# Performance work log

Hardware: AMD Instinct MI355X
Metric: run time of the kernel (lower is better)

Reference implementation:

```python
import jax, jax.numpy as jnp
import numpy as np

EEG_CH = 64      # eeg_channel_new
WIN = 128        # window_length
KEN = 10         # cnn_ken_num
CONV_H = 64      # cnn_conv_hight (stride/kernel height)


def setup_inputs() -> dict:
    key = jax.random.key(0)
    ks = jax.random.split(key, 11)
    n = jax.random.normal
    return {
        "x": n(ks[0], (1, 1, 66, 128), dtype=jnp.float32),
        # SE fcn: Linear(64,64) -> Tanh -> Linear(64,64) -> Sigmoid -> Softmax
        "se_w1": n(ks[1], (64, 64), dtype=jnp.float32) * 0.1,
        "se_b1": n(ks[2], (64,), dtype=jnp.float32) * 0.1,
        "se_w2": n(ks[3], (64, 64), dtype=jnp.float32) * 0.1,
        "se_b2": n(ks[4], (64,), dtype=jnp.float32) * 0.1,
        # Conv2d(1, 10, (64, 9), stride=(64, 1))
        "conv_w": n(ks[5], (10, 1, 64, 9), dtype=jnp.float32) * 0.05,
        "conv_b": n(ks[6], (10,), dtype=jnp.float32) * 0.05,
        # fcn: Linear(20,10) -> Sigmoid -> Linear(10,2) -> Softmax
        "fcn_w1": n(ks[7], (10, 20), dtype=jnp.float32) * 0.1,
        "fcn_b1": n(ks[8], (10,), dtype=jnp.float32) * 0.1,
        "fcn_w2": n(ks[9], (2, 10), dtype=jnp.float32) * 0.1,
        "fcn_b2": n(ks[10], (2,), dtype=jnp.float32) * 0.1,
    }


def _dot(a, b):
    # Faithful to torch: tensordot over dim 0 -> [64,1]; diag of non-square -> [1];
    # then broadcast-divide by per-column norms -> [64].
    temp = jnp.diagonal(jnp.tensordot(a, b, axes=[[0], [0]]))  # [1]
    norm_a = jnp.linalg.norm(a, axis=0)                        # [64]
    norm_b = jnp.linalg.norm(b, axis=0)                        # [1]
    return temp / (norm_a * norm_b)                            # [64]


def reference(x, se_w1, se_b1, se_w2, se_b2, conv_w, conv_b,
              fcn_w1, fcn_b1, fcn_w2, fcn_b2):
    eeg = x[:, :, 1:1 + EEG_CH, :]      # [1,1,64,128]
    wav_a = x[:, :, 0:1, :]             # [1,1,1,128]
    wav_b = x[:, :, -1:, :]             # [1,1,1,128]

    e2 = eeg.reshape(EEG_CH, WIN)       # [64,128]
    r_a = _dot(e2.T, wav_a.reshape(1, WIN).T)   # [64]
    r_b = _dot(e2.T, wav_b.reshape(1, WIN).T)   # [64]
    eeg_r = jnp.concatenate([r_a, r_b]).reshape(2, -1)  # [2,64]

    # SE channel attention
    h = jnp.tanh(eeg_r @ se_w1.T + se_b1)
    se_w = jax.nn.softmax(jax.nn.sigmoid(h @ se_w2.T + se_b2), axis=1)  # [2,64]
    sd = eeg.reshape(1, EEG_CH, WIN).transpose(1, 0, 2)  # [64,1,128]
    sd = jnp.concatenate([sd, sd], axis=0)               # [128,1,128]
    # (transpose(0,2) * w.view(1,-1)).transpose(0,2) == scale along doubled-channel dim
    eeg_se = (sd * se_w.reshape(-1)[:, None, None]).transpose(1, 0, 2)  # [1,128,128]

    y = eeg_se.reshape(1, 1, 2 * EEG_CH, WIN)            # [1,1,128,128]
    y = jax.lax.conv_general_dilated(
        y, conv_w, window_strides=(CONV_H, 1), padding='VALID',
        dimension_numbers=('NCHW', 'OIHW', 'NCHW'))       # [1,10,2,120]
    y = jax.nn.relu(y + conv_b[None, :, None, None])
    # AdaptiveAvgPool2d((2,1)): H already 2, mean over W
    y = jnp.mean(y, axis=3, keepdims=True)                # [1,10,2,1]
    y = y.reshape(1, -1)                                  # [1,20]

    h2 = jax.nn.sigmoid(y @ fcn_w1.T + fcn_b1)
    return jax.nn.softmax(h2 @ fcn_w2.T + fcn_b2, axis=1)  # [1,2]
```

## Files before the change

kernel.cpp:

```cpp
#include <hip/hip_runtime.h>
#include <math.h>

#define EEG_CH 64
#define WIN    128
#define KW     9
#define OUTW   120
#define NOUT   10
#define ROWP   132
#define CWP    12

__device__ float        g_msum[2 * NOUT];
__device__ unsigned int g_ctr = 0;

__device__ __forceinline__ float readlane_f(float v, int l) {
    return __int_as_float(__builtin_amdgcn_readlane(__float_as_int(v), l));
}

__launch_bounds__(1024)
__global__ void cnn_fused(const float* __restrict__ xg,
                          const float* __restrict__ w1g, const float* __restrict__ b1g,
                          const float* __restrict__ w2g, const float* __restrict__ b2g,
                          const float* __restrict__ cwg, const float* __restrict__ cbg,
                          const float* __restrict__ f1w, const float* __restrict__ f1b,
                          const float* __restrict__ f2w, const float* __restrict__ f2b,
                          float* __restrict__ out)
{
    __shared__ float w1l[64 * 64];
    __shared__ float w2l[64 * 64];
    __shared__ float xl[64 * ROWP];
    __shared__ float cwl[64 * CWP];
    __shared__ float rnorm[66];
    __shared__ float nums[2];
    __shared__ float sef[128];
    __shared__ float part[8][2][OUTW];
    __shared__ float msh[2];
    __shared__ int   sflag;
    __shared__ float msums[2 * NOUT];
    __shared__ float fcnl[232];

    const int tid  = threadIdx.x;
    const int wv   = tid >> 6;
    const int lane = tid & 63;
    const int o    = blockIdx.x;

    const int chbase = (wv & 7) * 8;

    if (tid < 576) {
        const float v = cwg[o * (EEG_CH * KW) + tid];
        cwl[(tid / KW) * CWP + (tid % KW)] = v;
    } else if (tid < 808) {
        const int t = tid - 576;
        float v;
        if      (t < 200) v = f1w[t];
        else if (t < 210) v = f1b[t - 200];
        else if (t < 230) v = f2w[t - 210];
        else              v = f2b[t - 230];
        fcnl[t] = v;
    }
    for (int t = tid; t < 2048; t += 1024) {
        const int row = t >> 5, c4 = t & 31;
        const float4 v = *(const float4*)(xg + (row + 1) * WIN + c4 * 4);
        *(float4*)(xl + row * ROWP + c4 * 4) = v;
    }
    for (int t = tid; t < 2048; t += 1024) {
        const int j  = t & 63;
        const int i4 = (t >> 6) & 15;
        const float* __restrict__ src = (t < 1024) ? w1g : w2g;
        float* __restrict__ dst = (t < 1024) ? w1l : w2l;
        const float4 v = *(const float4*)(src + j * 64 + i4 * 4);
        dst[(i4 * 4 + 0) * 64 + j] = v.x;
        dst[(i4 * 4 + 1) * 64 + j] = v.y;
        dst[(i4 * 4 + 2) * 64 + j] = v.z;
        dst[(i4 * 4 + 3) * 64 + j] = v.w;
    }
    for (int row = wv; row < 66; row += 16) {
        const float v0 = xg[row * WIN + lane];
        const float v1 = xg[row * WIN + 64 + lane];
        float s = v0 * v0 + v1 * v1;
        for (int off = 32; off > 0; off >>= 1) s += __shfl_xor(s, off, 64);
        if (lane == 0) rnorm[row] = sqrtf(s);
    }
    if (wv < 2) {
        const int wrow = (wv == 0) ? 0 : 65;
        float p = xg[WIN + lane]      * xg[wrow * WIN + lane]
                + xg[WIN + 64 + lane] * xg[wrow * WIN + 64 + lane];
        for (int off = 32; off > 0; off >>= 1) p += __shfl_xor(p, off, 64);
        if (lane == 0) nums[wv] = p;
    }
    __syncthreads();

    const int wbase = (lane < 60) ? 2 * lane : 116;
    float p0a[8], p1a[8];
    if (wv < 8) {
        #pragma unroll
        for (int ii = 0; ii < 8; ++ii) {
            const int i = chbase + ii;
            const float2* xp = (const float2*)(xl + i * ROWP + wbase);
            const float2 x0 = xp[0], x1 = xp[1], x2 = xp[2], x3 = xp[3], x4 = xp[4];
            const float xw[10] = { x0.x, x0.y, x1.x, x1.y, x2.x, x2.y,
                                   x3.x, x3.y, x4.x, x4.y };
            const float4 wa = *(const float4*)(cwl + i * CWP);
            const float4 wb = *(const float4*)(cwl + i * CWP + 4);
            const float  w8 = cwl[i * CWP + 8];
            const float wk[KW] = { wa.x, wa.y, wa.z, wa.w,
                                   wb.x, wb.y, wb.z, wb.w, w8 };
            float p0 = 0.f, p1 = 0.f;
            #pragma unroll
            for (int k = 0; k < KW; ++k) {
                p0 += xw[k]     * wk[k];
                p1 += xw[k + 1] * wk[k];
            }
            p0a[ii] = p0;
            p1a[ii] = p1;
        }
    } else if (wv < 10) {
        const int r = wv - 8, j = lane;
        const float er = nums[r] / (rnorm[j + 1] * (r == 0 ? rnorm[0] : rnorm[65]));
        float acc = b1g[j];
        #pragma unroll
        for (int i = 0; i < 64; ++i)
            acc += readlane_f(er, i) * w1l[i * 64 + j];
        const float hv = tanhf(acc);
        float acc2 = b2g[j];
        #pragma unroll
        for (int i = 0; i < 64; ++i)
            acc2 += readlane_f(hv, i) * w2l[i * 64 + j];
        const float sg = 1.f / (1.f + expf(-acc2));
        float mx = sg;
        for (int off = 32; off > 0; off >>= 1) mx = fmaxf(mx, __shfl_xor(mx, off, 64));
        const float e = expf(sg - mx);
        float ss = e;
        for (int off = 32; off > 0; off >>= 1) ss += __shfl_xor(ss, off, 64);
        sef[r * 64 + j] = e / ss;
    }
    __syncthreads();

    if (wv < 8) {
        float q00 = 0.f, q01 = 0.f;
        float q10 = 0.f, q11 = 0.f;
        #pragma unroll
        for (int ii = 0; ii < 8; ++ii) {
            const float s0 = sef[chbase + ii];
            const float s1 = sef[64 + chbase + ii];
            q00 += s0 * p0a[ii];  q01 += s0 * p1a[ii];
            q10 += s1 * p0a[ii];  q11 += s1 * p1a[ii];
        }
        if (lane < 60) {
            *(float2*)(&part[wv][0][wbase]) = make_float2(q00, q01);
            *(float2*)(&part[wv][1][wbase]) = make_float2(q10, q11);
        }
    }
    __syncthreads();

    if (wv < 2) {
        const float bo = cbg[o];
        float r = 0.f;
        if (lane < 60) {
            float v0 = part[0][wv][wbase], v1 = part[0][wv][wbase + 1];
            #pragma unroll
            for (int q = 1; q < 8; ++q) {
                v0 += part[q][wv][wbase];
                v1 += part[q][wv][wbase + 1];
            }
            v0 += bo; v1 += bo;
            r = fmaxf(v0, 0.f) + fmaxf(v1, 0.f);
        }
        for (int off = 32; off > 0; off >>= 1) r += __shfl_xor(r, off, 64);
        if (lane == 0) msh[wv] = r * (1.0f / OUTW);
    }
    __syncthreads();

    if (tid == 0) {
        __hip_atomic_store(&g_msum[o * 2 + 0], msh[0], __ATOMIC_RELAXED, __HIP_MEMORY_SCOPE_AGENT);
        __hip_atomic_store(&g_msum[o * 2 + 1], msh[1], __ATOMIC_RELAXED, __HIP_MEMORY_SCOPE_AGENT);
        const unsigned old = __hip_atomic_fetch_add(&g_ctr, 1u, __ATOMIC_ACQ_REL, __HIP_MEMORY_SCOPE_AGENT);
        sflag = (old % 10u == 9u) ? 1 : 0;
    }
    __syncthreads();

    if (sflag) {
        if (tid < 2 * NOUT)
            msums[tid] = __hip_atomic_load(&g_msum[tid], __ATOMIC_ACQUIRE, __HIP_MEMORY_SCOPE_AGENT);
        __syncthreads();
        if (tid < 64) {
            float h2v = 0.f;
            if (lane < 10) {
                float a = fcnl[200 + lane];
                #pragma unroll
                for (int p = 0; p < 20; ++p) a += msums[p] * fcnl[lane * 20 + p];
                h2v = 1.f / (1.f + expf(-a));
            }
            float t0 = (lane < 10) ? h2v * fcnl[210 + lane] : 0.f;
            float t1 = (lane < 10) ? h2v * fcnl[220 + lane] : 0.f;
            for (int off = 32; off > 0; off >>= 1) {
                t0 += __shfl_xor(t0, off, 64);
                t1 += __shfl_xor(t1, off, 64);
            }
            if (lane == 0) {
                const float l0 = fcnl[230] + t0, l1 = fcnl[231] + t1;
                const float m  = fmaxf(l0, l1);
                const float e0 = expf(l0 - m), e1 = expf(l1 - m);
                out[0] = e0 / (e0 + e1);
                out[1] = e1 / (e0 + e1);
            }
        }
    }
}

extern "C" void kernel_launch(void* const* d_in, const int* in_sizes, int n_in,
                              void* d_out, int out_size, void* d_ws, size_t ws_size,
                              hipStream_t stream) {
    (void)in_sizes; (void)n_in; (void)ws_size; (void)out_size; (void)d_ws;
    const float* xg  = (const float*)d_in[0];
    const float* w1  = (const float*)d_in[1];
    const float* b1  = (const float*)d_in[2];
    const float* w2  = (const float*)d_in[3];
    const float* b2  = (const float*)d_in[4];
    const float* cw  = (const float*)d_in[5];
    const float* cb  = (const float*)d_in[6];
    const float* f1w = (const float*)d_in[7];
    const float* f1b = (const float*)d_in[8];
    const float* f2w = (const float*)d_in[9];
    const float* f2b = (const float*)d_in[10];
    float* out = (float*)d_out;

    cnn_fused<<<dim3(NOUT), dim3(1024), 0, stream>>>(xg, w1, b1, w2, b2,
                                                     cw, cb, f1w, f1b, f2w, f2b, out);
}
```

Before: 82.90 us.

## Hold SE weights in registers and read conv input directly from global

The SE-branch waves now load their rows of the two 64x64 weight matrices straight into registers as float4s, so the transposed LDS staging of those matrices goes away. The conv waves read x windows directly from global or L1 instead of going through an LDS copy. Row-norm work is moved off the SE waves so their register loads can overlap it. Together these remove roughly 50KB of LDS traffic and staging stores, at the cost of 128 extra VGPRs per SE lane (possible spilling under the 1024-thread launch bound) and uncached-LDS global reads in the conv loop.

```diff
diff --git a/kernel.cpp b/kernel.cpp
--- a/kernel.cpp
+++ b/kernel.cpp
@@ -6,7 +6,6 @@
 #define KW     9
 #define OUTW   120
 #define NOUT   10
-#define ROWP   132
 #define CWP    12
 
 __device__ float        g_msum[2 * NOUT];
@@ -25,9 +24,6 @@
                           const float* __restrict__ f2w, const float* __restrict__ f2b,
                           float* __restrict__ out)
 {
-    __shared__ float w1l[64 * 64];
-    __shared__ float w2l[64 * 64];
-    __shared__ float xl[64 * ROWP];
     __shared__ float cwl[64 * CWP];
     __shared__ float rnorm[66];
     __shared__ float nums[2];
@@ -45,11 +41,24 @@
 
     const int chbase = (wv & 7) * 8;
 
-    if (tid < 576) {
-        const float v = cwg[o * (EEG_CH * KW) + tid];
-        cwl[(tid / KW) * CWP + (tid % KW)] = v;
-    } else if (tid < 808) {
-        const int t = tid - 576;
+    float4 w1r[16], w2r[16];
+    float  b1v = 0.f, b2v = 0.f;
+    if (wv == 8 || wv == 9) {
+        const float* __restrict__ r1 = w1g + lane * 64;
+        const float* __restrict__ r2 = w2g + lane * 64;
+        #pragma unroll
+        for (int q = 0; q < 16; ++q) w1r[q] = *(const float4*)(r1 + 4 * q);
+        #pragma unroll
+        for (int q = 0; q < 16; ++q) w2r[q] = *(const float4*)(r2 + 4 * q);
+        b1v = b1g[lane];
+        b2v = b2g[lane];
+    }
+    if (wv < 8) {
+        for (int t = tid; t < 576; t += 512)
+            cwl[(t / KW) * CWP + (t % KW)] = cwg[o * (EEG_CH * KW) + t];
+    }
+    if (tid >= 640 && tid < 872) {
+        const int t = tid - 640;
         float v;
         if      (t < 200) v = f1w[t];
         else if (t < 210) v = f1b[t - 200];
@@ -57,28 +66,15 @@
         else              v = f2b[t - 230];
         fcnl[t] = v;
     }
-    for (int t = tid; t < 2048; t += 1024) {
-        const int row = t >> 5, c4 = t & 31;
-        const float4 v = *(const float4*)(xg + (row + 1) * WIN + c4 * 4);
-        *(float4*)(xl + row * ROWP + c4 * 4) = v;
-    }
-    for (int t = tid; t < 2048; t += 1024) {
-        const int j  = t & 63;
-        const int i4 = (t >> 6) & 15;
-        const float* __restrict__ src = (t < 1024) ? w1g : w2g;
-        float* __restrict__ dst = (t < 1024) ? w1l : w2l;
-        const float4 v = *(const float4*)(src + j * 64 + i4 * 4);
-        dst[(i4 * 4 + 0) * 64 + j] = v.x;
-        dst[(i4 * 4 + 1) * 64 + j] = v.y;
-        dst[(i4 * 4 + 2) * 64 + j] = v.z;
-        dst[(i4 * 4 + 3) * 64 + j] = v.w;
-    }
-    for (int row = wv; row < 66; row += 16) {
-        const float v0 = xg[row * WIN + lane];
-        const float v1 = xg[row * WIN + 64 + lane];
-        float s = v0 * v0 + v1 * v1;
-        for (int off = 32; off > 0; off >>= 1) s += __shfl_xor(s, off, 64);
-        if (lane == 0) rnorm[row] = sqrtf(s);
+    if (wv < 8 || wv >= 10) {
+        const int wvn = (wv < 8) ? wv : wv - 2;
+        for (int row = wvn; row < 66; row += 14) {
+            const float v0 = xg[row * WIN + lane];
+            const float v1 = xg[row * WIN + 64 + lane];
+            float s = v0 * v0 + v1 * v1;
+            for (int off = 32; off > 0; off >>= 1) s += __shfl_xor(s, off, 64);
+            if (lane == 0) rnorm[row] = sqrtf(s);
+        }
     }
     if (wv < 2) {
         const int wrow = (wv == 0) ? 0 : 65;
@@ -95,7 +91,7 @@
         #pragma unroll
         for (int ii = 0; ii < 8; ++ii) {
             const int i = chbase + ii;
-            const float2* xp = (const float2*)(xl + i * ROWP + wbase);
+            const float2* xp = (const float2*)(xg + (i + 1) * WIN + wbase);
             const float2 x0 = xp[0], x1 = xp[1], x2 = xp[2], x3 = xp[3], x4 = xp[4];
             const float xw[10] = { x0.x, x0.y, x1.x, x1.y, x2.x, x2.y,
                                    x3.x, x3.y, x4.x, x4.y };
@@ -116,15 +112,25 @@
     } else if (wv < 10) {
         const int r = wv - 8, j = lane;
         const float er = nums[r] / (rnorm[j + 1] * (r == 0 ? rnorm[0] : rnorm[65]));
-        float acc = b1g[j];
-        #pragma unroll
-        for (int i = 0; i < 64; ++i)
-            acc += readlane_f(er, i) * w1l[i * 64 + j];
+        float acc = b1v;
+        #pragma unroll
+        for (int q = 0; q < 16; ++q) {
+            const float4 w = w1r[q];
+            acc += readlane_f(er, 4 * q + 0) * w.x;
+            acc += readlane_f(er, 4 * q + 1) * w.y;
+            acc += readlane_f(er, 4 * q + 2) * w.z;
+            acc += readlane_f(er, 4 * q + 3) * w.w;
+        }
         const float hv = tanhf(acc);
-        float acc2 = b2g[j];
-        #pragma unroll
-        for (int i = 0; i < 64; ++i)
-            acc2 += readlane_f(hv, i) * w2l[i * 64 + j];
+        float acc2 = b2v;
+        #pragma unroll
+        for (int q = 0; q < 16; ++q) {
+            const float4 w = w2r[q];
+            acc2 += readlane_f(hv, 4 * q + 0) * w.x;
+            acc2 += readlane_f(hv, 4 * q + 1) * w.y;
+            acc2 += readlane_f(hv, 4 * q + 2) * w.z;
+            acc2 += readlane_f(hv, 4 * q + 3) * w.w;
+        }
         const float sg = 1.f / (1.f + expf(-acc2));
         float mx = sg;
         for (int off = 32; off > 0; off >>= 1) mx = fmaxf(mx, __shfl_xor(mx, off, 64));
```

After: 89.42 us. 1.08x slower.
